# Kernel tuning notes

Measured on AMD Instinct MI355X. Metric: run time of the kernel, lower is better.

Reference implementation:

```python
import jax, jax.numpy as jnp
import numpy as np

B, L, C, K = 4, 32768, 64, 7
NORM_FACTOR = 1.0
EPS = 1e-5


def setup_inputs() -> dict:
    key = jax.random.key(0)
    ks = jax.random.split(key, 7)
    return {
        "x": jax.random.normal(ks[0], (B, L, C), jnp.float32),
        "weights": jax.random.normal(ks[1], (C, C, K), jnp.float32) * 0.05,  # ~lecun scale
        "w_conv": jax.random.normal(ks[2], (C, C), jnp.float32) * 0.125,
        "scale1": jax.random.uniform(ks[3], (C,), jnp.float32, 0.5, 1.5),
        "bias1": jax.random.normal(ks[4], (C,), jnp.float32) * 0.1,
        "scale2": jax.random.uniform(ks[5], (C,), jnp.float32, 0.5, 1.5),
        "bias2": jax.random.normal(ks[6], (C,), jnp.float32) * 0.1,
    }


def _batchnorm(x, scale, bias):
    # train-mode BatchNorm: stats over (batch, length), feature axis last
    mean = jnp.mean(x, axis=(0, 1), keepdims=True)
    var = jnp.var(x, axis=(0, 1), keepdims=True)
    return (x - mean) * jax.lax.rsqrt(var + EPS) * scale + bias


def reference(x, weights, w_conv, scale1, bias1, scale2, bias2):
    b, l, c = x.shape
    k = weights.shape[-1]
    x_ = x
    # unfold: windows of 2K at stride 2 -> (B, C*2K, T) -> (B, C, T, 2K)
    p = jax.lax.conv_general_dilated_patches(
        jnp.transpose(x, (0, 2, 1)), filter_shape=(2 * k,),
        window_strides=(2,), padding=((0, 0),))
    t = p.shape[-1]
    xp = jnp.transpose(jnp.reshape(p, (b, c, 2 * k, t)), (0, 1, 3, 2))
    # dynamic gate weights: (B, 2T, C) x (Cout, Cin, K) -> (B, Cout, 2T, K)
    w = jnp.einsum('blc,dck->bdlk', x_[:, -(2 * t):, :], weights)
    even_seq = w[:, :, ::2, :]   # (B, C, T, K)
    odd_seq = w[:, :, 1::2, :]   # (B, C, T, K)
    w = jnp.reshape(jnp.stack([even_seq, odd_seq], axis=-1), (b, c, t, 2 * k))
    w = jnp.tanh(w / NORM_FACTOR)
    y = jnp.sum(xp * w, axis=3)            # (B, C, T)
    y = jnp.transpose(y, (0, 2, 1))        # (B, T, C)
    y = x_[:, ::2, :][:, -t:, :] + y       # skip and inner_skip
    y = _batchnorm(y, scale1, bias1)
    y_ = y
    z = y @ w_conv                          # 1x1 conv, no bias
    z = _batchnorm(z, scale2, bias2)
    z = jax.nn.gelu(z)                      # approximate=True, matches flax default
    return y_ + z
```

## Files before the change

kernel.cpp:

```cpp
#include <hip/hip_runtime.h>
#include <hip/hip_bf16.h>

#define B_ 4
#define L_ 32768
#define C_ 64
#define K_ 7
#define T_ 16378
#define M_ (B_*T_)
#define TJ 16
#define IT 4
#define NJB 256
#define NBLKA (B_*NJB)
#define NBZ 512
#define NBE 1024

#define OF_WB   0
#define OF_WB2  14336
#define OF_Y    16384
#define OF_PS1  (OF_Y + M_*32)
#define OF_PQ1  (OF_PS1 + 64*NBLKA)
#define OF_PS2  (OF_PQ1 + 64*NBLKA)
#define OF_PQ2  (OF_PS2 + 64*NBZ)
#define OF_C1   (OF_PQ2 + 64*NBZ)
#define OF_C2   (OF_C1 + 128)

typedef __attribute__((ext_vector_type(8))) short short8;
typedef __attribute__((ext_vector_type(4))) float f32x4;

__device__ __forceinline__ unsigned cvt_pk_bf16(float a, float b) {
    unsigned r;
    asm("v_cvt_pk_bf16_f32 %0, %1, %2" : "=v"(r) : "v"(a), "v"(b));
    return r;
}

__device__ __forceinline__ float fast_tanh(float x) {
    float e = __builtin_amdgcn_exp2f(x * 2.885390082f);
    return __builtin_fmaf(-2.f, __builtin_amdgcn_rcpf(1.f + e), 1.f);
}

__device__ __forceinline__ float gelu_tanh(float v) {
    float u = 0.7978845608028654f * (v + 0.044715f * v * v * v);
    return 0.5f * v * (1.f + fast_tanh(u));
}

__device__ __forceinline__ float bfu(ushort h) {
    union { unsigned u; float f; } v; v.u = ((unsigned)h) << 16; return v.f;
}
__device__ __forceinline__ float bflo(unsigned p) {
    union { unsigned u; float f; } v; v.u = p << 16; return v.f;
}

__global__ void kPb(const float* __restrict__ w, ushort* __restrict__ Wb) {
    int i = blockIdx.x * 256 + threadIdx.x;
    if (i < 28672) {
        int j = i & 7;
        int l = (i >> 3) & 63;
        int q = i >> 9;
        int nt = q % 28, kt = q / 28;
        int k = kt * 32 + 8 * (l >> 4) + j;
        int n = nt * 16 + (l & 15);
        int d = n / 7, kk = n - 7 * d;
        Wb[i] = (ushort)(cvt_pk_bf16(w[(d * 64 + k) * 7 + kk], 0.f) & 0xffffu);
    }
}

__global__ __launch_bounds__(256, 4) void kA(const float* __restrict__ x,
                                             const ushort* __restrict__ Wb,
                                             ushort* __restrict__ y,
                                             float* __restrict__ ps,
                                             float* __restrict__ pq) {
    __shared__ char sm[4 * 7616 + 4 * 1496];

    const int tid = threadIdx.x;
    const int w = tid >> 6, l = tid & 63;
    char* gw  = sm + w * 7616;
    char* xpw = sm + 4 * 7616 + w * 1496;
    const int b = blockIdx.y;
    const float* xb = x + b * (L_ * 64);

    short8 wreg[7][2];
    #pragma unroll
    for (int i = 0; i < 7; ++i) {
        wreg[i][0] = *(const short8*)&Wb[((7 * w + i) * 64 + l) * 8];
        wreg[i][1] = *(const short8*)&Wb[((28 + 7 * w + i) * 64 + l) * 8];
    }

    const int cl = l & 15, r0 = 4 * (l >> 4);
    const int g = l >> 4, dp = l & 15;
    float S = 0.f, Q = 0.f;

    for (int it = 0; it < IT; ++it) {
        const int jt = blockIdx.x * IT + it;
        const int j0 = jt * TJ;
        const int xrow0 = 2 * j0;
        const bool tail = (jt == NJB * IT - 1);

        #pragma unroll
        for (int q = 0; q < 6; ++q) {
            int idx = q * 64 + l;
            int rp = idx >> 4, c = idx & 15;
            if (rp < 22) {
                int ra = xrow0 + 2 * rp, rb = ra + 1;
                if (tail) { ra = min(ra, L_ - 1); rb = min(rb, L_ - 1); }
                float va = xb[ra * 64 + 16 * w + c];
                float vb = xb[rb * 64 + 16 * w + c];
                *(unsigned*)(xpw + rp * 68 + c * 4) = cvt_pk_bf16(va, vb);
            }
        }

        short8 afr[2][2];
        #pragma unroll
        for (int mt = 0; mt < 2; ++mt)
            #pragma unroll
            for (int kt = 0; kt < 2; ++kt) {
                int row = xrow0 + 12 + mt * 16 + cl;
                if (tail) row = min(row, L_ - 1);
                const float* pr = xb + row * 64 + kt * 32 + (l >> 4) * 8;
                float4 v0 = *(const float4*)pr;
                float4 v1 = *(const float4*)(pr + 4);
                uint4 u;
                u.x = cvt_pk_bf16(v0.x, v0.y);
                u.y = cvt_pk_bf16(v0.z, v0.w);
                u.z = cvt_pk_bf16(v1.x, v1.y);
                u.w = cvt_pk_bf16(v1.z, v1.w);
                afr[mt][kt] = *(short8*)&u;
            }

        #pragma unroll
        for (int i = 0; i < 7; ++i) {
            f32x4 acc0 = {0.f, 0.f, 0.f, 0.f};
            f32x4 acc1 = {0.f, 0.f, 0.f, 0.f};
            acc0 = __builtin_amdgcn_mfma_f32_16x16x32_bf16(afr[0][0], wreg[i][0], acc0, 0, 0, 0);
            acc0 = __builtin_amdgcn_mfma_f32_16x16x32_bf16(afr[0][1], wreg[i][1], acc0, 0, 0, 0);
            acc1 = __builtin_amdgcn_mfma_f32_16x16x32_bf16(afr[1][0], wreg[i][0], acc1, 0, 0, 0);
            acc1 = __builtin_amdgcn_mfma_f32_16x16x32_bf16(afr[1][1], wreg[i][1], acc1, 0, 0, 0);
            char* base = gw + (i * 16 + cl) * 68 + r0 * 2;
            *(unsigned*)(base)      = cvt_pk_bf16(fast_tanh(acc0[0]), fast_tanh(acc0[1]));
            *(unsigned*)(base + 4)  = cvt_pk_bf16(fast_tanh(acc0[2]), fast_tanh(acc0[3]));
            *(unsigned*)(base + 32) = cvt_pk_bf16(fast_tanh(acc1[0]), fast_tanh(acc1[1]));
            *(unsigned*)(base + 36) = cvt_pk_bf16(fast_tanh(acc1[2]), fast_tanh(acc1[3]));
        }

        #pragma unroll
        for (int p = 0; p < 2; ++p) {
            const int jj0 = 2 * g + 8 * p;
            unsigned xv[8];
            #pragma unroll
            for (int k2 = 0; k2 < 8; ++k2)
                xv[k2] = *(const unsigned*)(xpw + (jj0 + k2) * 68 + dp * 4);
            float acc0 = bflo(xv[6]);
            float acc1 = bflo(xv[7]);
            const char* gb = gw + dp * 476 + jj0 * 4;
            #pragma unroll
            for (int kk = 0; kk < K_; ++kk) {
                unsigned g0 = *(const unsigned*)(gb + kk * 68);
                unsigned g1 = *(const unsigned*)(gb + kk * 68 + 4);
                asm("v_dot2_f32_bf16 %0, %1, %2, %0" : "+v"(acc0) : "v"(xv[kk]),     "v"(g0));
                asm("v_dot2_f32_bf16 %0, %1, %2, %0" : "+v"(acc1) : "v"(xv[kk + 1]), "v"(g1));
            }
            float o0 = __shfl_xor(acc0, 1);
            float o1 = __shfl_xor(acc1, 1);
            const int j = j0 + jj0;
            if (j < T_) {
                if ((dp & 1) == 0) {
                    *(unsigned*)((char*)y + (b * T_ + j) * 128 + (16 * w + dp) * 2)     = cvt_pk_bf16(acc0, o0);
                    *(unsigned*)((char*)y + (b * T_ + j + 1) * 128 + (16 * w + dp) * 2) = cvt_pk_bf16(acc1, o1);
                }
                S += acc0 + acc1;
                Q += acc0 * acc0 + acc1 * acc1;
            }
        }
    }

    S += __shfl_xor(S, 16); S += __shfl_xor(S, 32);
    Q += __shfl_xor(Q, 16); Q += __shfl_xor(Q, 32);
    if (l < 16) {
        int d = 16 * w + l;
        int blk = b * NJB + blockIdx.x;
        ps[d * NBLKA + blk] = S;
        pq[d * NBLKA + blk] = Q;
    }
}

__global__ void kB(const float* __restrict__ ps, const float* __restrict__ pq,
                   float* __restrict__ A, float* __restrict__ BB,
                   const float* __restrict__ scale, const float* __restrict__ bias,
                   int nblk, float invN) {
    const int c = blockIdx.x;
    const float* bs = ps + (long)c * nblk;
    const float* bq = pq + (long)c * nblk;
    float S = 0.f, Q = 0.f;
    for (int i = threadIdx.x; i < nblk; i += 256) {
        S += bs[i];
        Q += bq[i];
    }
    for (int o = 32; o > 0; o >>= 1) {
        S += __shfl_down(S, o);
        Q += __shfl_down(Q, o);
    }
    __shared__ float rs[4], rq[4];
    if ((threadIdx.x & 63) == 0) { rs[threadIdx.x >> 6] = S; rq[threadIdx.x >> 6] = Q; }
    __syncthreads();
    if (threadIdx.x == 0) {
        S = rs[0] + rs[1] + rs[2] + rs[3];
        Q = rq[0] + rq[1] + rq[2] + rq[3];
        float m = S * invN;
        float var = Q * invN - m * m;
        float rstd = rsqrtf(var + 1e-5f);
        float a = rstd * scale[c];
        A[c] = a;
        BB[c] = bias[c] - m * a;
    }
}

__global__ void kW(const float* __restrict__ wconv, const float* __restrict__ A1,
                   ushort* __restrict__ Wb2) {
    int i = blockIdx.x * 256 + threadIdx.x;
    if (i < 4096) {
        int j = i & 7, lane = (i >> 3) & 63, q2 = i >> 9;
        int kt = q2 >> 2, nt = q2 & 3;
        int c = kt * 32 + 8 * (lane >> 4) + j;
        int e = nt * 16 + (lane & 15);
        Wb2[i] = (ushort)(cvt_pk_bf16(A1[c] * wconv[c * 64 + e], 0.f) & 0xffffu);
    }
}

__global__ __launch_bounds__(256) void kZ(const ushort* __restrict__ y,
                                          const ushort* __restrict__ Wb2,
                                          float* __restrict__ ps2,
                                          float* __restrict__ pq2) {
    __shared__ float red[2][4][64];
    const int tid = threadIdx.x, w = tid >> 6, l = tid & 63;
    short8 bfr[4][2];
    #pragma unroll
    for (int nt = 0; nt < 4; ++nt)
        #pragma unroll
        for (int kt = 0; kt < 2; ++kt)
            bfr[nt][kt] = *(const short8*)&Wb2[((kt * 4 + nt) * 64 + l) * 8];

    float ss[4] = {0.f, 0.f, 0.f, 0.f}, qq[4] = {0.f, 0.f, 0.f, 0.f};
    #pragma unroll
    for (int g2 = 0; g2 < 2; ++g2) {
        long rowg = (long)blockIdx.x * 128 + g2 * 64 + w * 16 + (l & 15);
        short8 a0 = {0, 0, 0, 0, 0, 0, 0, 0};
        short8 a1 = {0, 0, 0, 0, 0, 0, 0, 0};
        if (rowg < M_) {
            const char* yr = (const char*)y + rowg * 128 + (l >> 4) * 16;
            a0 = *(const short8*)yr;
            a1 = *(const short8*)(yr + 64);
        }
        #pragma unroll
        for (int nt = 0; nt < 4; ++nt) {
            f32x4 acc = {0.f, 0.f, 0.f, 0.f};
            acc = __builtin_amdgcn_mfma_f32_16x16x32_bf16(a0, bfr[nt][0], acc, 0, 0, 0);
            acc = __builtin_amdgcn_mfma_f32_16x16x32_bf16(a1, bfr[nt][1], acc, 0, 0, 0);
            #pragma unroll
            for (int i = 0; i < 4; ++i) { ss[nt] += acc[i]; qq[nt] += acc[i] * acc[i]; }
        }
    }
    #pragma unroll
    for (int nt = 0; nt < 4; ++nt) {
        float s2 = ss[nt] + __shfl_xor(ss[nt], 16); s2 += __shfl_xor(s2, 32);
        float q2 = qq[nt] + __shfl_xor(qq[nt], 16); q2 += __shfl_xor(q2, 32);
        if (l < 16) { red[0][w][nt * 16 + l] = s2; red[1][w][nt * 16 + l] = q2; }
    }
    __syncthreads();
    if (tid < 64) {
        float S = red[0][0][tid] + red[0][1][tid] + red[0][2][tid] + red[0][3][tid];
        float Q = red[1][0][tid] + red[1][1][tid] + red[1][2][tid] + red[1][3][tid];
        ps2[tid * NBZ + blockIdx.x] = S;
        pq2[tid * NBZ + blockIdx.x] = Q;
    }
}

__global__ __launch_bounds__(256) void kE(const ushort* __restrict__ y,
                                          const ushort* __restrict__ Wb2,
                                          const float* __restrict__ A1,
                                          const float* __restrict__ B1,
                                          const float* __restrict__ A2,
                                          const float* __restrict__ B2,
                                          float* __restrict__ out) {
    __shared__ float zs[64][68];
    __shared__ float cf[4][64];
    const int tid = threadIdx.x, w = tid >> 6, l = tid & 63;

    if (tid < 64)       cf[0][tid] = A1[tid];
    else if (tid < 128) cf[1][tid - 64] = B1[tid - 64];
    else if (tid < 192) cf[2][tid - 128] = A2[tid - 128];
    else                cf[3][tid - 192] = B2[tid - 192];

    short8 bfr[4][2];
    #pragma unroll
    for (int nt = 0; nt < 4; ++nt)
        #pragma unroll
        for (int kt = 0; kt < 2; ++kt)
            bfr[nt][kt] = *(const short8*)&Wb2[((kt * 4 + nt) * 64 + l) * 8];

    const long row0 = (long)blockIdx.x * 64;
    long rowg = row0 + w * 16 + (l & 15);
    short8 a0 = {0, 0, 0, 0, 0, 0, 0, 0};
    short8 a1 = {0, 0, 0, 0, 0, 0, 0, 0};
    if (rowg < M_) {
        const char* yr = (const char*)y + rowg * 128 + (l >> 4) * 16;
        a0 = *(const short8*)yr;
        a1 = *(const short8*)(yr + 64);
    }
    #pragma unroll
    for (int nt = 0; nt < 4; ++nt) {
        f32x4 acc = {0.f, 0.f, 0.f, 0.f};
        acc = __builtin_amdgcn_mfma_f32_16x16x32_bf16(a0, bfr[nt][0], acc, 0, 0, 0);
        acc = __builtin_amdgcn_mfma_f32_16x16x32_bf16(a1, bfr[nt][1], acc, 0, 0, 0);
        const int e = nt * 16 + (l & 15);
        #pragma unroll
        for (int i = 0; i < 4; ++i)
            zs[w * 16 + 4 * (l >> 4) + i][e] = acc[i];
    }
    __syncthreads();

    #pragma unroll
    for (int i = 0; i < 4; ++i) {
        int rloc = i * 16 + (tid >> 4);
        long gr = row0 + rloc;
        int ch0 = (tid & 15) * 4;
        if (gr < M_) {
            uint2 yp = *(const uint2*)((const char*)y + gr * 128 + ch0 * 2);
            float4 z4 = *(const float4*)&zs[rloc][ch0];
            float yv0 = bflo(yp.x), yv1 = bfu((ushort)(yp.x >> 16));
            float yv2 = bflo(yp.y), yv3 = bfu((ushort)(yp.y >> 16));
            float4 o;
            o.x = fmaf(cf[0][ch0 + 0], yv0, cf[1][ch0 + 0]) + gelu_tanh(fmaf(cf[2][ch0 + 0], z4.x, cf[3][ch0 + 0]));
            o.y = fmaf(cf[0][ch0 + 1], yv1, cf[1][ch0 + 1]) + gelu_tanh(fmaf(cf[2][ch0 + 1], z4.y, cf[3][ch0 + 1]));
            o.z = fmaf(cf[0][ch0 + 2], yv2, cf[1][ch0 + 2]) + gelu_tanh(fmaf(cf[2][ch0 + 2], z4.z, cf[3][ch0 + 2]));
            o.w = fmaf(cf[0][ch0 + 3], yv3, cf[1][ch0 + 3]) + gelu_tanh(fmaf(cf[2][ch0 + 3], z4.w, cf[3][ch0 + 3]));
            *(float4*)&out[gr * 64 + ch0] = o;
        }
    }
}

extern "C" void kernel_launch(void* const* d_in, const int* in_sizes, int n_in,
                              void* d_out, int out_size, void* d_ws, size_t ws_size,
                              hipStream_t stream) {
    const float* x       = (const float*)d_in[0];
    const float* weights = (const float*)d_in[1];
    const float* w_conv  = (const float*)d_in[2];
    const float* scale1  = (const float*)d_in[3];
    const float* bias1   = (const float*)d_in[4];
    const float* scale2  = (const float*)d_in[5];
    const float* bias2   = (const float*)d_in[6];
    float* out = (float*)d_out;
    float* ws  = (float*)d_ws;

    ushort* Wb  = (ushort*)(ws + OF_WB);
    ushort* Wb2 = (ushort*)(ws + OF_WB2);
    ushort* yb  = (ushort*)(ws + OF_Y);
    float* ps1 = ws + OF_PS1;
    float* pq1 = ws + OF_PQ1;
    float* ps2 = ws + OF_PS2;
    float* pq2 = ws + OF_PQ2;
    float* A1  = ws + OF_C1;
    float* BB1 = ws + OF_C1 + 64;
    float* A2  = ws + OF_C2;
    float* BB2 = ws + OF_C2 + 64;

    const float invN = 1.f / (float)M_;

    kPb<<<112, 256, 0, stream>>>(weights, Wb);
    kA<<<dim3(NJB, B_), 256, 0, stream>>>(x, Wb, yb, ps1, pq1);
    kB<<<64, 256, 0, stream>>>(ps1, pq1, A1, BB1, scale1, bias1, NBLKA, invN);
    kW<<<16, 256, 0, stream>>>(w_conv, A1, Wb2);
    kZ<<<NBZ, 256, 0, stream>>>(yb, Wb2, ps2, pq2);
    kB<<<64, 256, 0, stream>>>(ps2, pq2, A2, BB2, scale2, bias2, NBZ, invN);
    kE<<<NBE, 256, 0, stream>>>(yb, Wb2, A1, BB1, A2, BB2, out);
}
```

Measured before the change: 56.79 us.

## Drop LDS x staging in kA, double its grid, fuse kW into kB

kA no longer stages x pairs into shared memory. Each lane reads its 16 rows of x directly from global memory, in fp32, and packs them to bf16 in registers. This frees LDS, so the launch-bounds occupancy hint goes from 4 to 5, and each block now handles 2 tiles instead of 4 across twice as many blocks. The gate values are read with one 64-bit LDS load instead of two 32-bit loads. The separate kW launch is folded into the first kB reduction, which removes one kernel launch. The cost is strided, uncoalesced per-channel global reads of x, which may lean on the cache.

Result: slower. 70.09 us (+23.4%).

```diff
diff --git a/kernel.cpp b/kernel.cpp
--- a/kernel.cpp
+++ b/kernel.cpp
@@ -8,8 +8,8 @@
 #define T_ 16378
 #define M_ (B_*T_)
 #define TJ 16
-#define IT 4
-#define NJB 256
+#define IT 2
+#define NJB 512
 #define NBLKA (B_*NJB)
 #define NBZ 512
 #define NBE 1024
@@ -64,17 +64,16 @@
     }
 }
 
-__global__ __launch_bounds__(256, 4) void kA(const float* __restrict__ x,
+__global__ __launch_bounds__(256, 5) void kA(const float* __restrict__ x,
                                              const ushort* __restrict__ Wb,
                                              ushort* __restrict__ y,
                                              float* __restrict__ ps,
                                              float* __restrict__ pq) {
-    __shared__ char sm[4 * 7616 + 4 * 1496];
+    __shared__ char sm[4 * 7616];
 
     const int tid = threadIdx.x;
     const int w = tid >> 6, l = tid & 63;
-    char* gw  = sm + w * 7616;
-    char* xpw = sm + 4 * 7616 + w * 1496;
+    char* gw = sm + w * 7616;
     const int b = blockIdx.y;
     const float* xb = x + b * (L_ * 64);
 
@@ -87,6 +86,7 @@
 
     const int cl = l & 15, r0 = 4 * (l >> 4);
     const int g = l >> 4, dp = l & 15;
+    const int ch = 16 * w + dp;
     float S = 0.f, Q = 0.f;
 
     for (int it = 0; it < IT; ++it) {
@@ -94,19 +94,6 @@
         const int j0 = jt * TJ;
         const int xrow0 = 2 * j0;
         const bool tail = (jt == NJB * IT - 1);
-
-        #pragma unroll
-        for (int q = 0; q < 6; ++q) {
-            int idx = q * 64 + l;
-            int rp = idx >> 4, c = idx & 15;
-            if (rp < 22) {
-                int ra = xrow0 + 2 * rp, rb = ra + 1;
-                if (tail) { ra = min(ra, L_ - 1); rb = min(rb, L_ - 1); }
-                float va = xb[ra * 64 + 16 * w + c];
-                float vb = xb[rb * 64 + 16 * w + c];
-                *(unsigned*)(xpw + rp * 68 + c * 4) = cvt_pk_bf16(va, vb);
-            }
-        }
 
         short8 afr[2][2];
         #pragma unroll
@@ -144,27 +131,34 @@
         #pragma unroll
         for (int p = 0; p < 2; ++p) {
             const int jj0 = 2 * g + 8 * p;
+            const int rbase = xrow0 + 2 * jj0;
+            float xr[16];
+            #pragma unroll
+            for (int r = 0; r < 16; ++r) {
+                int row = rbase + r;
+                if (tail) row = min(row, L_ - 1);
+                xr[r] = xb[row * 64 + ch];
+            }
             unsigned xv[8];
             #pragma unroll
             for (int k2 = 0; k2 < 8; ++k2)
-                xv[k2] = *(const unsigned*)(xpw + (jj0 + k2) * 68 + dp * 4);
-            float acc0 = bflo(xv[6]);
-            float acc1 = bflo(xv[7]);
+                xv[k2] = cvt_pk_bf16(xr[2 * k2], xr[2 * k2 + 1]);
+            float acc0 = xr[12];
+            float acc1 = xr[14];
             const char* gb = gw + dp * 476 + jj0 * 4;
             #pragma unroll
             for (int kk = 0; kk < K_; ++kk) {
-                unsigned g0 = *(const unsigned*)(gb + kk * 68);
-                unsigned g1 = *(const unsigned*)(gb + kk * 68 + 4);
-                asm("v_dot2_f32_bf16 %0, %1, %2, %0" : "+v"(acc0) : "v"(xv[kk]),     "v"(g0));
-                asm("v_dot2_f32_bf16 %0, %1, %2, %0" : "+v"(acc1) : "v"(xv[kk + 1]), "v"(g1));
+                uint2 gp = *(const uint2*)(gb + kk * 68);
+                asm("v_dot2_f32_bf16 %0, %1, %2, %0" : "+v"(acc0) : "v"(xv[kk]),     "v"(gp.x));
+                asm("v_dot2_f32_bf16 %0, %1, %2, %0" : "+v"(acc1) : "v"(xv[kk + 1]), "v"(gp.y));
             }
             float o0 = __shfl_xor(acc0, 1);
             float o1 = __shfl_xor(acc1, 1);
             const int j = j0 + jj0;
             if (j < T_) {
                 if ((dp & 1) == 0) {
-                    *(unsigned*)((char*)y + (b * T_ + j) * 128 + (16 * w + dp) * 2)     = cvt_pk_bf16(acc0, o0);
-                    *(unsigned*)((char*)y + (b * T_ + j + 1) * 128 + (16 * w + dp) * 2) = cvt_pk_bf16(acc1, o1);
+                    *(unsigned*)((char*)y + (b * T_ + j) * 128 + ch * 2)     = cvt_pk_bf16(acc0, o0);
+                    *(unsigned*)((char*)y + (b * T_ + j + 1) * 128 + ch * 2) = cvt_pk_bf16(acc1, o1);
                 }
                 S += acc0 + acc1;
                 Q += acc0 * acc0 + acc1 * acc1;
@@ -185,7 +179,8 @@
 __global__ void kB(const float* __restrict__ ps, const float* __restrict__ pq,
                    float* __restrict__ A, float* __restrict__ BB,
                    const float* __restrict__ scale, const float* __restrict__ bias,
-                   int nblk, float invN) {
+                   int nblk, float invN,
+                   const float* __restrict__ wconv, ushort* __restrict__ Wb2) {
     const int c = blockIdx.x;
     const float* bs = ps + (long)c * nblk;
     const float* bq = pq + (long)c * nblk;
@@ -199,6 +194,7 @@
         Q += __shfl_down(Q, o);
     }
     __shared__ float rs[4], rq[4];
+    __shared__ float sa;
     if ((threadIdx.x & 63) == 0) { rs[threadIdx.x >> 6] = S; rq[threadIdx.x >> 6] = Q; }
     __syncthreads();
     if (threadIdx.x == 0) {
@@ -210,18 +206,18 @@
         float a = rstd * scale[c];
         A[c] = a;
         BB[c] = bias[c] - m * a;
-    }
-}
-
-__global__ void kW(const float* __restrict__ wconv, const float* __restrict__ A1,
-                   ushort* __restrict__ Wb2) {
-    int i = blockIdx.x * 256 + threadIdx.x;
-    if (i < 4096) {
-        int j = i & 7, lane = (i >> 3) & 63, q2 = i >> 9;
-        int kt = q2 >> 2, nt = q2 & 3;
-        int c = kt * 32 + 8 * (lane >> 4) + j;
-        int e = nt * 16 + (lane & 15);
-        Wb2[i] = (ushort)(cvt_pk_bf16(A1[c] * wconv[c * 64 + e], 0.f) & 0xffffu);
+        sa = a;
+    }
+    if (Wb2 != nullptr) {
+        __syncthreads();
+        if (threadIdx.x < 64) {
+            int e = threadIdx.x;
+            float wv = sa * wconv[c * 64 + e];
+            int kt = c >> 5, rem = c & 31, bslot = rem >> 3, j = rem & 7;
+            int lane = bslot * 16 + (e & 15), nt = e >> 4;
+            Wb2[(((kt * 4 + nt) * 64 + lane) << 3) + j] =
+                (ushort)(cvt_pk_bf16(wv, 0.f) & 0xffffu);
+        }
     }
 }
 
@@ -366,9 +362,8 @@
 
     kPb<<<112, 256, 0, stream>>>(weights, Wb);
     kA<<<dim3(NJB, B_), 256, 0, stream>>>(x, Wb, yb, ps1, pq1);
-    kB<<<64, 256, 0, stream>>>(ps1, pq1, A1, BB1, scale1, bias1, NBLKA, invN);
-    kW<<<16, 256, 0, stream>>>(w_conv, A1, Wb2);
+    kB<<<64, 256, 0, stream>>>(ps1, pq1, A1, BB1, scale1, bias1, NBLKA, invN, w_conv, Wb2);
     kZ<<<NBZ, 256, 0, stream>>>(yb, Wb2, ps2, pq2);
-    kB<<<64, 256, 0, stream>>>(ps2, pq2, A2, BB2, scale2, bias2, NBZ, invN);
+    kB<<<64, 256, 0, stream>>>(ps2, pq2, A2, BB2, scale2, bias2, NBZ, invN, nullptr, nullptr);
     kE<<<NBE, 256, 0, stream>>>(yb, Wb2, A1, BB1, A2, BB2, out);
 }
```
